# Optimization experiments

Measured on AMD Instinct MI355X. Metric: run time of the kernel, lower is better.

Reference implementation:

```python
import math
import jax, jax.numpy as jnp
import numpy as np

B, T, C, H = 16, 512, 1024, 16
HD = C // H
EPS = 1e-5

def new_gelu(x):
    return 0.5 * x * (1.0 + jnp.tanh(math.sqrt(2.0 / math.pi) * (x + 0.044715 * x ** 3)))

def layer_norm(x, g, b):
    mu = jnp.mean(x, axis=-1, keepdims=True)
    var = jnp.mean((x - mu) ** 2, axis=-1, keepdims=True)
    return (x - mu) * jax.lax.rsqrt(var + EPS) * g + b

def setup_inputs() -> dict:
    key = jax.random.key(0)
    ks = jax.random.split(key, 12)
    s = 0.02
    return {
        "x": jax.random.normal(ks[0], (B, T, C), jnp.float32),
        "attention_mask": jnp.ones((B, T), jnp.int32),
        "ln1_g": jnp.ones((C,), jnp.float32),
        "ln1_b": jnp.zeros((C,), jnp.float32),
        "w_attn": jax.random.normal(ks[1], (C, 3 * C), jnp.float32) * s,
        "b_attn": jnp.zeros((3 * C,), jnp.float32),
        "w_o": jax.random.normal(ks[2], (C, C), jnp.float32) * s,
        "b_o": jnp.zeros((C,), jnp.float32),
        "ln2_g": jnp.ones((C,), jnp.float32),
        "ln2_b": jnp.zeros((C,), jnp.float32),
        "w_fc": jax.random.normal(ks[3], (C, 4 * C), jnp.float32) * s,
        "b_fc": jnp.zeros((4 * C,), jnp.float32),
        "w_fc2": jax.random.normal(ks[4], (4 * C, C), jnp.float32) * s,
        "b_fc2": jnp.zeros((C,), jnp.float32),
    }

def reference(x, attention_mask, ln1_g, ln1_b, w_attn, b_attn, w_o, b_o, ln2_g, ln2_b, w_fc, b_fc, w_fc2, b_fc2):
    # --- self-attention on ln_1(x) ---
    h = layer_norm(x, ln1_g, ln1_b)
    qkv = h @ w_attn + b_attn                      # [B,T,3C]
    q, k, v = jnp.split(qkv, 3, axis=-1)
    q = q.reshape(B, T, H, HD).transpose(0, 2, 1, 3)  # [B,H,T,HD]
    k = k.reshape(B, T, H, HD).transpose(0, 2, 1, 3)
    v = v.reshape(B, T, H, HD).transpose(0, 2, 1, 3)
    att = jnp.einsum("bhqd,bhkd->bhqk", q, k) * (1.0 / math.sqrt(HD))
    mask = attention_mask[:, None, None, :]        # [B,1,1,T]
    att = jnp.where(mask == 0, -jnp.inf, att)
    att = jax.nn.softmax(att, axis=-1)
    y = jnp.einsum("bhqk,bhkd->bhqd", att, v)      # [B,H,T,HD]
    y = y.transpose(0, 2, 1, 3).reshape(B, T, C)
    x = x + (y @ w_o + b_o)
    # --- MLP on ln_2(x) ---
    h2 = layer_norm(x, ln2_g, ln2_b)
    x = x + (new_gelu(h2 @ w_fc + b_fc) @ w_fc2 + b_fc2)
    return x
```

## Files before the change

### kernel.cpp

```cpp
#include <hip/hip_runtime.h>
#include <math.h>
#include <stdint.h>

#define BB 16
#define TT 512
#define CC 1024
#define HH 16
#define HD 64
#define NT (BB*TT)

typedef __bf16 bf16x8 __attribute__((ext_vector_type(8)));
typedef float f32x4 __attribute__((ext_vector_type(4)));

__device__ __forceinline__ unsigned short f2bf(float x) {
    union { float f; unsigned u; } v; v.f = x;
    unsigned r = v.u + 0x7fffu + ((v.u >> 16) & 1u);
    return (unsigned short)(r >> 16);
}

__device__ __forceinline__ void gload_lds16(const void* g, void* l) {
    __builtin_amdgcn_global_load_lds((const __attribute__((address_space(1))) uint32_t*)g,
                                     (__attribute__((address_space(3))) uint32_t*)l, 16, 0, 0);
}

__global__ __launch_bounds__(256) void tcvt_kernel(const float* __restrict__ in,
                                                   unsigned short* __restrict__ out,
                                                   int K, int N) {
    __shared__ float Tt[32][33];
    int n0 = blockIdx.x * 32, k0 = blockIdx.y * 32;
    int t = threadIdx.x;
#pragma unroll
    for (int i = 0; i < 4; i++) {
        int idx = i * 256 + t; int r = idx >> 5, c = idx & 31;
        Tt[r][c] = in[(size_t)(k0 + r) * N + n0 + c];
    }
    __syncthreads();
#pragma unroll
    for (int i = 0; i < 4; i++) {
        int idx = i * 256 + t; int r = idx >> 5, c = idx & 31;
        out[(size_t)(n0 + r) * K + k0 + c] = f2bf(Tt[c][r]);
    }
}

__global__ __launch_bounds__(256) void ln_kernel(const float* __restrict__ x,
                                                 const float* __restrict__ g,
                                                 const float* __restrict__ b,
                                                 unsigned short* __restrict__ out) {
    int row = blockIdx.x;
    const float* xr = x + (size_t)row * CC;
    unsigned short* orow = out + (size_t)row * CC;
    int tid = threadIdx.x;
    float v[4];
    float lsum = 0.f, lsq = 0.f;
#pragma unroll
    for (int i = 0; i < 4; i++) {
        v[i] = xr[tid + 256 * i];
        lsum += v[i];
        lsq  += v[i] * v[i];
    }
    __shared__ float ssum[4], ssq[4];
#pragma unroll
    for (int o = 32; o > 0; o >>= 1) {
        lsum += __shfl_down(lsum, o);
        lsq  += __shfl_down(lsq, o);
    }
    int wid = tid >> 6, lane = tid & 63;
    if (lane == 0) { ssum[wid] = lsum; ssq[wid] = lsq; }
    __syncthreads();
    if (tid == 0) {
        float s = 0.f, q = 0.f;
#pragma unroll
        for (int i = 0; i < 4; i++) { s += ssum[i]; q += ssq[i]; }
        float mu = s / CC;
        float var = q / CC - mu * mu;
        ssum[0] = mu;
        ssq[0] = rsqrtf(var + 1e-5f);
    }
    __syncthreads();
    float mu = ssum[0], rstd = ssq[0];
#pragma unroll
    for (int i = 0; i < 4; i++) {
        int c = tid + 256 * i;
        orow[c] = f2bf((v[i] - mu) * rstd * g[c] + b[c]);
    }
}

enum { EPI_BIAS_RES_F32 = 1, EPI_BIAS_GELU_BF16 = 2, EPI_QKV = 3 };

template <int EPI>
__global__ __launch_bounds__(256) void mgemm(const unsigned short* __restrict__ A,
                                             const unsigned short* __restrict__ Bt,
                                             const float* __restrict__ bias,
                                             const float* __restrict__ R,
                                             float* __restrict__ Cf,
                                             unsigned short* __restrict__ Cb,
                                             unsigned short* __restrict__ Vb,
                                             int M, int N, int K) {
    __shared__ __align__(16) unsigned short As[128 * 32];
    __shared__ __align__(16) unsigned short Bs[128 * 32];
    int tid = threadIdx.x;
    int w = tid >> 6, lane = tid & 63;
    int bm = blockIdx.y * 128, bn = blockIdx.x * 128;
    int wr = (w >> 1) * 64, wc = (w & 1) * 64;

    int kswz = ((tid & 3) ^ ((tid >> 3) & 3)) * 8;
    const unsigned short* gA0 = A + (size_t)(bm + (tid >> 2)) * K + kswz;
    const unsigned short* gA1 = A + (size_t)(bm + 64 + (tid >> 2)) * K + kswz;
    const unsigned short* gB0 = Bt + (size_t)(bn + (tid >> 2)) * K + kswz;
    const unsigned short* gB1 = Bt + (size_t)(bn + 64 + (tid >> 2)) * K + kswz;
    char* lA0 = (char*)As + w * 1024;
    char* lA1 = (char*)As + 4096 + w * 1024;
    char* lB0 = (char*)Bs + w * 1024;
    char* lB1 = (char*)Bs + 4096 + w * 1024;

    int ml = lane & 15, quad = lane >> 4;
    int rswz = quad ^ ((ml >> 1) & 3);
    const bf16x8* As8 = (const bf16x8*)As;
    const bf16x8* Bs8 = (const bf16x8*)Bs;
    const bf16x8* pa = As8 + (wr + ml) * 4 + rswz;
    const bf16x8* pb = Bs8 + (wc + ml) * 4 + rswz;

    f32x4 acc[4][4] = {};

    for (int k0 = 0; k0 < K; k0 += 32) {
        gload_lds16(gA0 + k0, lA0);
        gload_lds16(gA1 + k0, lA1);
        gload_lds16(gB0 + k0, lB0);
        gload_lds16(gB1 + k0, lB1);
        __syncthreads();
        bf16x8 a[4], bb[4];
#pragma unroll
        for (int ti = 0; ti < 4; ti++) a[ti] = pa[ti * 64];
#pragma unroll
        for (int tj = 0; tj < 4; tj++) bb[tj] = pb[tj * 64];
#pragma unroll
        for (int ti = 0; ti < 4; ti++)
#pragma unroll
            for (int tj = 0; tj < 4; tj++)
                acc[ti][tj] = __builtin_amdgcn_mfma_f32_16x16x32_bf16(a[ti], bb[tj], acc[ti][tj], 0, 0, 0);
        __syncthreads();
    }

#pragma unroll
    for (int ti = 0; ti < 4; ti++) {
#pragma unroll
        for (int tj = 0; tj < 4; tj++) {
            int n = bn + wc + tj * 16 + ml;
            int mbase = bm + wr + ti * 16 + quad * 4;
            float bv = bias[n];
            if (EPI == EPI_QKV && n >= 2 * CC) {
                int d = n & (HD - 1), hh = (n - 2 * CC) >> 6;
                int tok = mbase & (TT - 1), bi = mbase >> 9;
                ushort4 pk;
                pk.x = f2bf(acc[ti][tj][0] + bv);
                pk.y = f2bf(acc[ti][tj][1] + bv);
                pk.z = f2bf(acc[ti][tj][2] + bv);
                pk.w = f2bf(acc[ti][tj][3] + bv);
                *(ushort4*)&Vb[((size_t)(bi * HH + hh) * HD + d) * TT + tok] = pk;
            } else {
#pragma unroll
                for (int reg = 0; reg < 4; reg++) {
                    int m = mbase + reg;
                    float v = acc[ti][tj][reg] + bv;
                    if (EPI == EPI_BIAS_GELU_BF16) {
                        float u2 = 1.5957691216057308f * (v + 0.044715f * v * v * v);
                        v = v / (1.0f + __expf(-u2));
                        Cb[(size_t)m * N + n] = f2bf(v);
                    } else if (EPI == EPI_QKV) {
                        Cb[(size_t)m * N + n] = f2bf(v);
                    } else {
                        v += R[(size_t)m * N + n];
                        Cf[(size_t)m * N + n] = v;
                    }
                }
            }
        }
    }
}

__global__ __launch_bounds__(256) void attn_kernel(const unsigned short* __restrict__ qkvb,
                                                   const unsigned short* __restrict__ vt,
                                                   const int* __restrict__ mask,
                                                   unsigned short* __restrict__ yb) {
    __shared__ __align__(16) unsigned short Qs[64][72];
    __shared__ __align__(16) unsigned short Ks[64][72];
    __shared__ __align__(16) unsigned short Vs[64][72];
    __shared__ __align__(16) unsigned short Ps[4][16][72];
    __shared__ int ms[64];
    int qt = blockIdx.x, h = blockIdx.y, b = blockIdx.z;
    int tid = threadIdx.x;
    int w = tid >> 6, lane = tid & 63, ml = lane & 15, quad = lane >> 4;

    const size_t row3 = 3 * CC;
    const unsigned short* qbase = qkvb + (size_t)(b * TT + qt * 64) * row3 + h * HD;
    const unsigned short* kbase = qkvb + (size_t)(b * TT) * row3 + CC + h * HD;
    const unsigned short* vbase = vt + (size_t)(b * HH + h) * HD * TT;

#pragma unroll
    for (int i = 0; i < 2; i++) {
        int c = i * 256 + tid; int r = c >> 3, c8 = c & 7;
        *(uint4*)&Qs[r][c8 * 8] = *(const uint4*)(qbase + (size_t)r * row3 + c8 * 8);
    }

    f32x4 o[4] = {};
    float m_i[4], l_i[4];
#pragma unroll
    for (int r = 0; r < 4; r++) { m_i[r] = -1e30f; l_i[r] = 0.f; }

    for (int k0 = 0; k0 < TT; k0 += 64) {
#pragma unroll
        for (int i = 0; i < 2; i++) {
            int c = i * 256 + tid; int r = c >> 3, c8 = c & 7;
            *(uint4*)&Ks[r][c8 * 8] = *(const uint4*)(kbase + (size_t)(k0 + r) * row3 + c8 * 8);
            *(uint4*)&Vs[r][c8 * 8] = *(const uint4*)(vbase + (size_t)r * TT + k0 + c8 * 8);
        }
        if (tid < 64) ms[tid] = mask[b * TT + k0 + tid];
        __syncthreads();

        bf16x8 aq0 = *(const bf16x8*)&Qs[w * 16 + ml][quad * 8];
        bf16x8 aq1 = *(const bf16x8*)&Qs[w * 16 + ml][32 + quad * 8];
        float p[4][4];
        float mt[4] = {-1e30f, -1e30f, -1e30f, -1e30f};
#pragma unroll
        for (int tj = 0; tj < 4; tj++) {
            bf16x8 b0 = *(const bf16x8*)&Ks[tj * 16 + ml][quad * 8];
            bf16x8 b1 = *(const bf16x8*)&Ks[tj * 16 + ml][32 + quad * 8];
            f32x4 z = {};
            z = __builtin_amdgcn_mfma_f32_16x16x32_bf16(aq0, b0, z, 0, 0, 0);
            z = __builtin_amdgcn_mfma_f32_16x16x32_bf16(aq1, b1, z, 0, 0, 0);
            bool dead = (ms[tj * 16 + ml] == 0);
#pragma unroll
            for (int r = 0; r < 4; r++) {
                float v = dead ? -1e30f : z[r] * 0.125f;
                p[tj][r] = v;
                mt[r] = fmaxf(mt[r], v);
            }
        }
#pragma unroll
        for (int off = 1; off < 16; off <<= 1)
#pragma unroll
            for (int r = 0; r < 4; r++) mt[r] = fmaxf(mt[r], __shfl_xor(mt[r], off));
        float alpha[4], rs[4];
#pragma unroll
        for (int r = 0; r < 4; r++) {
            float mn = fmaxf(m_i[r], mt[r]);
            alpha[r] = __expf(m_i[r] - mn);
            m_i[r] = mn;
            rs[r] = 0.f;
#pragma unroll
            for (int tj = 0; tj < 4; tj++) {
                float e = __expf(p[tj][r] - mn);
                p[tj][r] = e;
                rs[r] += e;
            }
        }
#pragma unroll
        for (int off = 1; off < 16; off <<= 1)
#pragma unroll
            for (int r = 0; r < 4; r++) rs[r] += __shfl_xor(rs[r], off);
#pragma unroll
        for (int r = 0; r < 4; r++) {
            l_i[r] = l_i[r] * alpha[r] + rs[r];
#pragma unroll
            for (int tj = 0; tj < 4; tj++) o[tj][r] *= alpha[r];
        }
#pragma unroll
        for (int tj = 0; tj < 4; tj++)
#pragma unroll
            for (int r = 0; r < 4; r++)
                Ps[w][quad * 4 + r][tj * 16 + ml] = f2bf(p[tj][r]);
        bf16x8 pa0 = *(const bf16x8*)&Ps[w][ml][quad * 8];
        bf16x8 pa1 = *(const bf16x8*)&Ps[w][ml][32 + quad * 8];
#pragma unroll
        for (int tj = 0; tj < 4; tj++) {
            bf16x8 v0 = *(const bf16x8*)&Vs[tj * 16 + ml][quad * 8];
            bf16x8 v1 = *(const bf16x8*)&Vs[tj * 16 + ml][32 + quad * 8];
            o[tj] = __builtin_amdgcn_mfma_f32_16x16x32_bf16(pa0, v0, o[tj], 0, 0, 0);
            o[tj] = __builtin_amdgcn_mfma_f32_16x16x32_bf16(pa1, v1, o[tj], 0, 0, 0);
        }
        __syncthreads();
    }

#pragma unroll
    for (int r = 0; r < 4; r++) {
        float inv = 1.f / l_i[r];
        int q = qt * 64 + w * 16 + quad * 4 + r;
        unsigned short* yr = yb + (size_t)(b * TT + q) * CC + h * HD;
#pragma unroll
        for (int tj = 0; tj < 4; tj++)
            yr[tj * 16 + ml] = f2bf(o[tj][r] * inv);
    }
}

extern "C" void kernel_launch(void* const* d_in, const int* in_sizes, int n_in,
                              void* d_out, int out_size, void* d_ws, size_t ws_size,
                              hipStream_t stream) {
    const float* x      = (const float*)d_in[0];
    const int*   mask   = (const int*)d_in[1];
    const float* ln1_g  = (const float*)d_in[2];
    const float* ln1_b  = (const float*)d_in[3];
    const float* w_attn = (const float*)d_in[4];
    const float* b_attn = (const float*)d_in[5];
    const float* w_o    = (const float*)d_in[6];
    const float* b_o    = (const float*)d_in[7];
    const float* ln2_g  = (const float*)d_in[8];
    const float* ln2_b  = (const float*)d_in[9];
    const float* w_fc   = (const float*)d_in[10];
    const float* b_fc   = (const float*)d_in[11];
    const float* w_fc2  = (const float*)d_in[12];
    const float* b_fc2  = (const float*)d_in[13];
    float* out = (float*)d_out;

    char* ws = (char*)d_ws;
    size_t off = 0;
    unsigned short* wt_attn = (unsigned short*)(ws + off); off += (size_t)3 * CC * CC * 2;
    unsigned short* wt_o    = (unsigned short*)(ws + off); off += (size_t)CC * CC * 2;
    unsigned short* wt_fc   = (unsigned short*)(ws + off); off += (size_t)4 * CC * CC * 2;
    unsigned short* wt_fc2  = (unsigned short*)(ws + off); off += (size_t)4 * CC * CC * 2;
    unsigned short* qkvb    = (unsigned short*)(ws + off);
    unsigned short* act     = (unsigned short*)(ws + off); off += (size_t)NT * 3 * CC * 2;
    unsigned short* vt      = (unsigned short*)(ws + off); off += (size_t)BB * CC * TT * 2;
    unsigned short* hb      = (unsigned short*)(ws + off);
    unsigned short* yb      = (unsigned short*)(ws + off); off += (size_t)NT * CC * 2;
    float* x1               = (float*)(ws + off); off += (size_t)NT * CC * 4;
    unsigned short* h2b     = (unsigned short*)(ws + off); off += (size_t)NT * CC * 2;

    tcvt_kernel<<<dim3(3 * CC / 32, CC / 32), 256, 0, stream>>>(w_attn, wt_attn, CC, 3 * CC);
    tcvt_kernel<<<dim3(CC / 32, CC / 32), 256, 0, stream>>>(w_o, wt_o, CC, CC);
    tcvt_kernel<<<dim3(4 * CC / 32, CC / 32), 256, 0, stream>>>(w_fc, wt_fc, CC, 4 * CC);
    tcvt_kernel<<<dim3(CC / 32, 4 * CC / 32), 256, 0, stream>>>(w_fc2, wt_fc2, 4 * CC, CC);

    ln_kernel<<<NT, 256, 0, stream>>>(x, ln1_g, ln1_b, hb);
    mgemm<EPI_QKV><<<dim3(3 * CC / 128, NT / 128), 256, 0, stream>>>(
        hb, wt_attn, b_attn, nullptr, nullptr, qkvb, vt, NT, 3 * CC, CC);
    attn_kernel<<<dim3(TT / 64, HH, BB), 256, 0, stream>>>(qkvb, vt, mask, yb);
    mgemm<EPI_BIAS_RES_F32><<<dim3(CC / 128, NT / 128), 256, 0, stream>>>(
        yb, wt_o, b_o, x, x1, nullptr, nullptr, NT, CC, CC);
    ln_kernel<<<NT, 256, 0, stream>>>(x1, ln2_g, ln2_b, h2b);
    mgemm<EPI_BIAS_GELU_BF16><<<dim3(4 * CC / 128, NT / 128), 256, 0, stream>>>(
        h2b, wt_fc, b_fc, nullptr, nullptr, act, nullptr, NT, 4 * CC, CC);
    mgemm<EPI_BIAS_RES_F32><<<dim3(CC / 128, NT / 128), 256, 0, stream>>>(
        act, wt_fc2, b_fc2, x1, out, nullptr, nullptr, NT, CC, 4 * CC);
}
```

Before: 545.6 us.

## Double GEMM K-tile to 64 and add grouped block rasterization

The shared GEMM kernel now stages a K-slice of 64 per iteration instead of 32, with a matching 8-way XOR swizzle for LDS, so each iteration does twice the MFMA work per pair of barriers. Block indices are also remapped so groups of 8 row tiles walk across columns together, aiming for better L2 reuse of the weight and activation tiles. This halves the number of synchronizations and global-load issue rounds. The cost is doubled LDS use per block and more in-flight loads, which may reduce occupancy.

```diff
diff --git a/kernel.cpp b/kernel.cpp
--- a/kernel.cpp
+++ b/kernel.cpp
@@ -96,48 +96,64 @@
                                              unsigned short* __restrict__ Cb,
                                              unsigned short* __restrict__ Vb,
                                              int M, int N, int K) {
-    __shared__ __align__(16) unsigned short As[128 * 32];
-    __shared__ __align__(16) unsigned short Bs[128 * 32];
+    __shared__ __align__(16) unsigned short As[128 * 64];
+    __shared__ __align__(16) unsigned short Bs[128 * 64];
     int tid = threadIdx.x;
     int w = tid >> 6, lane = tid & 63;
-    int bm = blockIdx.y * 128, bn = blockIdx.x * 128;
+
+    int bid = blockIdx.y * gridDim.x + blockIdx.x;
+    int per = 8 * gridDim.x;
+    int grp = bid / per, rem = bid % per;
+    int bm = (grp * 8 + (rem & 7)) * 128;
+    int bn = (rem >> 3) * 128;
     int wr = (w >> 1) * 64, wc = (w & 1) * 64;
 
-    int kswz = ((tid & 3) ^ ((tid >> 3) & 3)) * 8;
-    const unsigned short* gA0 = A + (size_t)(bm + (tid >> 2)) * K + kswz;
-    const unsigned short* gA1 = A + (size_t)(bm + 64 + (tid >> 2)) * K + kswz;
-    const unsigned short* gB0 = Bt + (size_t)(bn + (tid >> 2)) * K + kswz;
-    const unsigned short* gB1 = Bt + (size_t)(bn + 64 + (tid >> 2)) * K + kswz;
-    char* lA0 = (char*)As + w * 1024;
-    char* lA1 = (char*)As + 4096 + w * 1024;
-    char* lB0 = (char*)Bs + w * 1024;
-    char* lB1 = (char*)Bs + 4096 + w * 1024;
+    int row8 = tid >> 3;
+    int kswz = ((tid & 7) ^ (row8 & 7)) * 8;
+    const unsigned short* gA = A + (size_t)(bm + row8) * K + kswz;
+    const unsigned short* gB = Bt + (size_t)(bn + row8) * K + kswz;
+    char* lA = (char*)As + w * 1024;
+    char* lB = (char*)Bs + w * 1024;
 
     int ml = lane & 15, quad = lane >> 4;
-    int rswz = quad ^ ((ml >> 1) & 3);
-    const bf16x8* As8 = (const bf16x8*)As;
-    const bf16x8* Bs8 = (const bf16x8*)Bs;
-    const bf16x8* pa = As8 + (wr + ml) * 4 + rswz;
-    const bf16x8* pb = Bs8 + (wc + ml) * 4 + rswz;
+    int s0 = ((quad ^ (ml & 7))) * 8;
+    int s1 = (((quad + 4) ^ (ml & 7))) * 8;
+    const unsigned short* rowA = As + (size_t)(wr + ml) * 64;
+    const unsigned short* rowB = Bs + (size_t)(wc + ml) * 64;
 
     f32x4 acc[4][4] = {};
 
-    for (int k0 = 0; k0 < K; k0 += 32) {
-        gload_lds16(gA0 + k0, lA0);
-        gload_lds16(gA1 + k0, lA1);
-        gload_lds16(gB0 + k0, lB0);
-        gload_lds16(gB1 + k0, lB1);
+    for (int k0 = 0; k0 < K; k0 += 64) {
+#pragma unroll
+        for (int p = 0; p < 4; p++) {
+            gload_lds16(gA + (size_t)(p * 32) * K + k0, lA + p * 4096);
+            gload_lds16(gB + (size_t)(p * 32) * K + k0, lB + p * 4096);
+        }
         __syncthreads();
-        bf16x8 a[4], bb[4];
-#pragma unroll
-        for (int ti = 0; ti < 4; ti++) a[ti] = pa[ti * 64];
-#pragma unroll
-        for (int tj = 0; tj < 4; tj++) bb[tj] = pb[tj * 64];
-#pragma unroll
-        for (int ti = 0; ti < 4; ti++)
-#pragma unroll
-            for (int tj = 0; tj < 4; tj++)
-                acc[ti][tj] = __builtin_amdgcn_mfma_f32_16x16x32_bf16(a[ti], bb[tj], acc[ti][tj], 0, 0, 0);
+        {
+            bf16x8 a[4], bb[4];
+#pragma unroll
+            for (int ti = 0; ti < 4; ti++) a[ti] = *(const bf16x8*)&rowA[ti * 1024 + s0];
+#pragma unroll
+            for (int tj = 0; tj < 4; tj++) bb[tj] = *(const bf16x8*)&rowB[tj * 1024 + s0];
+#pragma unroll
+            for (int ti = 0; ti < 4; ti++)
+#pragma unroll
+                for (int tj = 0; tj < 4; tj++)
+                    acc[ti][tj] = __builtin_amdgcn_mfma_f32_16x16x32_bf16(a[ti], bb[tj], acc[ti][tj], 0, 0, 0);
+        }
+        {
+            bf16x8 a[4], bb[4];
+#pragma unroll
+            for (int ti = 0; ti < 4; ti++) a[ti] = *(const bf16x8*)&rowA[ti * 1024 + s1];
+#pragma unroll
+            for (int tj = 0; tj < 4; tj++) bb[tj] = *(const bf16x8*)&rowB[tj * 1024 + s1];
+#pragma unroll
+            for (int ti = 0; ti < 4; ti++)
+#pragma unroll
+                for (int tj = 0; tj < 4; tj++)
+                    acc[ti][tj] = __builtin_amdgcn_mfma_f32_16x16x32_bf16(a[ti], bb[tj], acc[ti][tj], 0, 0, 0);
+        }
         __syncthreads();
     }
 
```

After: 520.5 us. 1.05x faster.

## Double-buffer LDS tiles in bf16 GEMM to overlap loads with MFMA

Applied to the files above, without the earlier changes.

The GEMM kernel now keeps two LDS buffers for A and B and issues the global-to-LDS loads for the next k-slice before running the MFMAs on the current one. The loop is unrolled by two so the buffers alternate without index arithmetic. The aim is to hide global load latency behind compute, which the single-buffer load/sync/compute loop exposed. It doubles LDS use per block, which may reduce occupancy, and it assumes K is a multiple of 64.

```diff
diff --git a/kernel.cpp b/kernel.cpp
--- a/kernel.cpp
+++ b/kernel.cpp
@@ -96,8 +96,8 @@
                                              unsigned short* __restrict__ Cb,
                                              unsigned short* __restrict__ Vb,
                                              int M, int N, int K) {
-    __shared__ __align__(16) unsigned short As[128 * 32];
-    __shared__ __align__(16) unsigned short Bs[128 * 32];
+    __shared__ __align__(16) unsigned short As[2][128 * 32];
+    __shared__ __align__(16) unsigned short Bs[2][128 * 32];
     int tid = threadIdx.x;
     int w = tid >> 6, lane = tid & 63;
     int bm = blockIdx.y * 128, bn = blockIdx.x * 128;
@@ -108,38 +108,49 @@
     const unsigned short* gA1 = A + (size_t)(bm + 64 + (tid >> 2)) * K + kswz;
     const unsigned short* gB0 = Bt + (size_t)(bn + (tid >> 2)) * K + kswz;
     const unsigned short* gB1 = Bt + (size_t)(bn + 64 + (tid >> 2)) * K + kswz;
-    char* lA0 = (char*)As + w * 1024;
-    char* lA1 = (char*)As + 4096 + w * 1024;
-    char* lB0 = (char*)Bs + w * 1024;
-    char* lB1 = (char*)Bs + 4096 + w * 1024;
 
     int ml = lane & 15, quad = lane >> 4;
     int rswz = quad ^ ((ml >> 1) & 3);
-    const bf16x8* As8 = (const bf16x8*)As;
-    const bf16x8* Bs8 = (const bf16x8*)Bs;
-    const bf16x8* pa = As8 + (wr + ml) * 4 + rswz;
-    const bf16x8* pb = Bs8 + (wc + ml) * 4 + rswz;
 
     f32x4 acc[4][4] = {};
 
-    for (int k0 = 0; k0 < K; k0 += 32) {
-        gload_lds16(gA0 + k0, lA0);
-        gload_lds16(gA1 + k0, lA1);
-        gload_lds16(gB0 + k0, lB0);
-        gload_lds16(gB1 + k0, lB1);
+#define STAGE(buf, k0)                                                  \
+    do {                                                                \
+        gload_lds16(gA0 + (k0), (char*)As[buf] + w * 1024);             \
+        gload_lds16(gA1 + (k0), (char*)As[buf] + 4096 + w * 1024);      \
+        gload_lds16(gB0 + (k0), (char*)Bs[buf] + w * 1024);             \
+        gload_lds16(gB1 + (k0), (char*)Bs[buf] + 4096 + w * 1024);      \
+    } while (0)
+
+#define COMPUTE(buf)                                                    \
+    do {                                                                \
+        const bf16x8* pa = (const bf16x8*)As[buf] + (wr + ml) * 4 + rswz; \
+        const bf16x8* pb = (const bf16x8*)Bs[buf] + (wc + ml) * 4 + rswz; \
+        bf16x8 a[4], bb[4];                                             \
+        _Pragma("unroll")                                               \
+        for (int ti = 0; ti < 4; ti++) a[ti] = pa[ti * 64];             \
+        _Pragma("unroll")                                               \
+        for (int tj = 0; tj < 4; tj++) bb[tj] = pb[tj * 64];            \
+        _Pragma("unroll")                                               \
+        for (int ti = 0; ti < 4; ti++)                                  \
+            _Pragma("unroll")                                           \
+            for (int tj = 0; tj < 4; tj++)                              \
+                acc[ti][tj] = __builtin_amdgcn_mfma_f32_16x16x32_bf16(  \
+                    a[ti], bb[tj], acc[ti][tj], 0, 0, 0);               \
+    } while (0)
+
+    STAGE(0, 0);
+    __syncthreads();
+    for (int k0 = 0; k0 < K; k0 += 64) {
+        if (k0 + 32 < K) STAGE(1, k0 + 32);
+        COMPUTE(0);
         __syncthreads();
-        bf16x8 a[4], bb[4];
-#pragma unroll
-        for (int ti = 0; ti < 4; ti++) a[ti] = pa[ti * 64];
-#pragma unroll
-        for (int tj = 0; tj < 4; tj++) bb[tj] = pb[tj * 64];
-#pragma unroll
-        for (int ti = 0; ti < 4; ti++)
-#pragma unroll
-            for (int tj = 0; tj < 4; tj++)
-                acc[ti][tj] = __builtin_amdgcn_mfma_f32_16x16x32_bf16(a[ti], bb[tj], acc[ti][tj], 0, 0, 0);
+        if (k0 + 64 < K) STAGE(0, k0 + 64);
+        COMPUTE(1);
         __syncthreads();
     }
+#undef STAGE
+#undef COMPUTE
 
 #pragma unroll
     for (int ti = 0; ti < 4; ti++) {
```

Result: faster. 515.1 us (-5.6%).
